# Kernel tuning notes

Hardware: AMD Instinct MI355X
Metric: run time of the kernel (lower is better)

The kernel has to match this reference:

```python
import jax, jax.numpy as jnp
import numpy as np

WS = 8          # window size
N = WS * WS     # tokens per window (64)
C = 256         # embed dim
H = 8           # heads
D = C // H      # head dim (32)
NW = 256        # windows per image
B_ = 2048       # total windows in batch (8 images * 256 windows)
CPB_HIDDEN = 512


def _make_relative_position_index():
    coords_h = np.arange(WS)
    coords_w = np.arange(WS)
    coords = np.stack(np.meshgrid(coords_h, coords_w, indexing='ij'))  # [2,WS,WS]
    coords = coords.reshape(2, -1)                                     # [2,N]
    rel = coords[:, :, None] - coords[:, None, :]                      # [2,N,N]
    rel = rel.transpose(1, 2, 0).astype(np.int64)                      # [N,N,2]
    rel[:, :, 0] += WS - 1
    rel[:, :, 1] += WS - 1
    rel[:, :, 0] *= 2 * WS - 1
    return rel.sum(-1)                                                 # [N,N]


def _make_relative_coords_table():
    rh = np.arange(-(WS - 1), WS, dtype=np.float64)
    rw = np.arange(-(WS - 1), WS, dtype=np.float64)
    tbl = np.stack(np.meshgrid(rh, rw, indexing='ij')).transpose(1, 2, 0)[None]  # [1,2W-1,2W-1,2]
    tbl[:, :, :, 0] /= (WS - 1)  # pretrained_window_size == window_size
    tbl[:, :, :, 1] /= (WS - 1)
    tbl *= 8
    tbl = np.sign(tbl) * np.log2(np.abs(tbl) + 1.0) / np.log2(8)
    return tbl.astype(np.float32)


def setup_inputs() -> dict:
    key = jax.random.key(0)
    ks = jax.random.split(key, 8)
    x = jax.random.normal(ks[0], (B_, N, C), dtype=jnp.float32)
    # shifted-window style additive mask: 0 for allowed, -100 for masked
    mask_bits = jax.random.uniform(ks[1], (NW, N, N)) < 0.1
    mask = jnp.where(mask_bits, jnp.float32(-100.0), jnp.float32(0.0))
    qkv_w = jax.random.normal(ks[2], (C, 3 * C), dtype=jnp.float32) * (1.0 / np.sqrt(C))
    q_bias = jnp.zeros((C,), jnp.float32)
    v_bias = jnp.zeros((C,), jnp.float32)
    logit_scale = jnp.full((H, 1, 1), np.log(10.0), dtype=jnp.float32)
    coords_table = jnp.asarray(_make_relative_coords_table())
    mlp1_w = jax.random.normal(ks[3], (2, CPB_HIDDEN), dtype=jnp.float32) * 0.5
    mlp1_b = jnp.zeros((CPB_HIDDEN,), jnp.float32)
    mlp2_w = jax.random.normal(ks[4], (CPB_HIDDEN, H), dtype=jnp.float32) * (1.0 / np.sqrt(CPB_HIDDEN))
    proj_w = jax.random.normal(ks[5], (C, C), dtype=jnp.float32) * (1.0 / np.sqrt(C))
    proj_b = jnp.zeros((C,), jnp.float32)
    rel_pos_index = jnp.asarray(_make_relative_position_index())  # [N,N] int64
    return {
        'x': x, 'mask': mask, 'qkv_w': qkv_w, 'q_bias': q_bias, 'v_bias': v_bias,
        'logit_scale': logit_scale, 'coords_table': coords_table,
        'mlp1_w': mlp1_w, 'mlp1_b': mlp1_b, 'mlp2_w': mlp2_w,
        'proj_w': proj_w, 'proj_b': proj_b, 'rel_pos_index': rel_pos_index,
    }


def _l2norm(t, axis=-1, eps=1e-12):
    n = jnp.sqrt(jnp.sum(t * t, axis=axis, keepdims=True))
    return t / jnp.maximum(n, eps)


def reference(x, mask, qkv_w, q_bias, v_bias, logit_scale, coords_table,
              mlp1_w, mlp1_b, mlp2_w, proj_w, proj_b, rel_pos_index):
    b, n, c = x.shape
    # qkv projection with (q_bias, 0, v_bias)
    qkv_bias = jnp.concatenate([q_bias, jnp.zeros_like(v_bias), v_bias], axis=0)
    qkv = x @ qkv_w + qkv_bias                          # [b, n, 3c]
    qkv = qkv.reshape(b, n, 3, H, D).transpose(2, 0, 3, 1, 4)  # [3, b, H, n, D]
    q, k, v = qkv[0], qkv[1], qkv[2]
    # cosine attention with learned per-head logit scale
    attn = jnp.einsum('bhnd,bhmd->bhnm', _l2norm(q), _l2norm(k))
    scale = jnp.exp(jnp.minimum(logit_scale, jnp.float32(np.log(1.0 / 0.01))))  # [H,1,1]
    attn = attn * scale[None]                           # [b, H, n, n]
    # continuous position bias MLP
    hbt = jax.nn.relu(coords_table @ mlp1_w + mlp1_b)   # [1, 2W-1, 2W-1, 512]
    bias_table = (hbt @ mlp2_w).reshape(-1, H)          # [(2W-1)^2, H]
    rel_bias = bias_table[rel_pos_index.reshape(-1)].reshape(n, n, H)
    rel_bias = 16.0 * jax.nn.sigmoid(rel_bias.transpose(2, 0, 1))  # [H, n, n]
    attn = attn + rel_bias[None]
    # shifted-window mask
    nw = mask.shape[0]
    attn = attn.reshape(b // nw, nw, H, n, n) + mask[None, :, None]
    attn = attn.reshape(b, H, n, n)
    attn = jax.nn.softmax(attn, axis=-1)
    out = jnp.einsum('bhnm,bhmd->bnhd', attn, v).reshape(b, n, c)
    return out @ proj_w + proj_b
```

## Files before the change

kernel.cpp:

```cpp
#include <hip/hip_runtime.h>
#include <hip/hip_bf16.h>
#include <stdint.h>

#define NTOK   64
#define CDIM   256
#define NHEAD  8
#define DHEAD  32
#define NWIN   256
#define BWIN   2048
#define MROWS  131072

typedef __attribute__((ext_vector_type(8))) short short8;
typedef __attribute__((ext_vector_type(4))) float f32x4;

__device__ __forceinline__ ushort f2bf(float f) {
  uint32_t u = __float_as_uint(f);
  u += 0x7fffu + ((u >> 16) & 1u);
  return (ushort)(u >> 16);
}
__device__ __forceinline__ void unpack8(uint4 u, float* f) {
  f[0] = __uint_as_float(u.x << 16);
  f[1] = __uint_as_float(u.x & 0xffff0000u);
  f[2] = __uint_as_float(u.y << 16);
  f[3] = __uint_as_float(u.y & 0xffff0000u);
  f[4] = __uint_as_float(u.z << 16);
  f[5] = __uint_as_float(u.z & 0xffff0000u);
  f[6] = __uint_as_float(u.w << 16);
  f[7] = __uint_as_float(u.w & 0xffff0000u);
}


__global__ void k_cast_bf16(const float* __restrict__ src, ushort* __restrict__ dst, int n4) {
  int i = blockIdx.x * blockDim.x + threadIdx.x;
  int stride = gridDim.x * blockDim.x;
  for (; i < n4; i += stride) {
    float4 v = ((const float4*)src)[i];
    ushort4 o;
    o.x = f2bf(v.x); o.y = f2bf(v.y); o.z = f2bf(v.z); o.w = f2bf(v.w);
    ((ushort4*)dst)[i] = o;
  }
}

__global__ void k_transpose_bf16(const float* __restrict__ src, ushort* __restrict__ dst, int K, int N) {
  int idx = blockIdx.x * 256 + threadIdx.x;
  if (idx < N * K) {
    int n = idx / K, k = idx - n * K;
    dst[idx] = f2bf(src[(size_t)k * N + n]);
  }
}

__global__ void k_cpb(const float* __restrict__ ct, const float* __restrict__ w1,
                      const float* __restrict__ b1, const float* __restrict__ w2,
                      float* __restrict__ out) {
  int p = blockIdx.x, t = threadIdx.x;
  float c0 = ct[p * 2], c1 = ct[p * 2 + 1];
  float acc[8];
#pragma unroll
  for (int h = 0; h < 8; ++h) acc[h] = 0.f;
  for (int j = t; j < 512; j += 256) {
    float hj = fmaxf(0.f, fmaf(c0, w1[j], fmaf(c1, w1[512 + j], b1[j])));
#pragma unroll
    for (int h = 0; h < 8; ++h) acc[h] = fmaf(hj, w2[j * 8 + h], acc[h]);
  }
#pragma unroll
  for (int off = 1; off < 64; off <<= 1)
#pragma unroll
    for (int h = 0; h < 8; ++h) acc[h] += __shfl_xor(acc[h], off, 64);
  __shared__ float red[4][8];
  if ((t & 63) == 0)
#pragma unroll
    for (int h = 0; h < 8; ++h) red[t >> 6][h] = acc[h];
  __syncthreads();
  if (t < 8) out[p * 8 + t] = red[0][t] + red[1][t] + red[2][t] + red[3][t];
}

__global__ void k_relbC(const float* __restrict__ bt, const int* __restrict__ rpi,
                        float* __restrict__ out) {
  int idx = blockIdx.x * 256 + threadIdx.x;
  int reg = idx & 3, l16 = (idx >> 2) & 15, g = (idx >> 6) & 3;
  int mt = (idx >> 8) & 3, nt = (idx >> 10) & 3, h = idx >> 12;
  int q = mt * 16 + l16, k = nt * 16 + g * 4 + reg;
  float v = bt[rpi[q * 64 + k] * 8 + h];
  out[idx] = 16.0f / (1.0f + __expf(-v));
}

__global__ void k_maskBits(const float* __restrict__ mask, unsigned char* __restrict__ out) {
  int idx = blockIdx.x * 256 + threadIdx.x;
  int b = idx & 15;
  int q6 = (idx >> 4) & 63;
  int wi = idx >> 10;
  int nt = b >> 2, mt = b & 3, g = q6 >> 4, l16 = q6 & 15;
  unsigned char v = 0;
#pragma unroll
  for (int reg = 0; reg < 4; ++reg) {
    int q = mt * 16 + l16, k = nt * 16 + g * 4 + reg;
    if (mask[(size_t)wi * 4096 + q * 64 + k] == 0.0f) v |= (unsigned char)(1 << reg);
  }
  out[idx] = v;
}

template <int MODE>
__global__ __launch_bounds__(256, 2) void gemm_bt(const ushort* __restrict__ A,
                                                  const ushort* __restrict__ BT,
                                                  void* __restrict__ Cout,
                                                  const float* __restrict__ bias0,
                                                  const float* __restrict__ bias1,
                                                  int K, int N) {
  __shared__ ushort As[128 * 64];
  __shared__ ushort Bs[128 * 64];
  const int t = threadIdx.x;
  const int bn = blockIdx.x, bm = blockIdx.y;
  const int wv = t >> 6, lane = t & 63, quad = lane >> 4, l16 = lane & 15;
  const int mbase = (wv & 1) * 64, nbase = (wv >> 1) * 64;

  f32x4 acc[4][4] = {};

  const int nkt = K >> 6;
  for (int kt = 0; kt < nkt; ++kt) {
    __syncthreads();
#pragma unroll
    for (int i = 0; i < 4; ++i) {
      int idx = i * 256 + t;
      int m = idx >> 3, c = idx & 7;
      int sw = (m * 8 + (c ^ (m & 7))) * 8;
      *(uint4*)(As + sw) = *(const uint4*)(A + (size_t)(bm * 128 + m) * K + kt * 64 + c * 8);
      *(uint4*)(Bs + sw) = *(const uint4*)(BT + (size_t)(bn * 128 + m) * K + kt * 64 + c * 8);
    }
    __syncthreads();
#pragma unroll
    for (int k2 = 0; k2 < 2; ++k2) {
      const int cidx = (k2 * 4 + quad) ^ (l16 & 7);
      short8 a[4], b[4];
#pragma unroll
      for (int mt = 0; mt < 4; ++mt)
        a[mt] = *(const short8*)(As + ((mbase + mt * 16 + l16) * 8 + cidx) * 8);
#pragma unroll
      for (int nt = 0; nt < 4; ++nt)
        b[nt] = *(const short8*)(Bs + ((nbase + nt * 16 + l16) * 8 + cidx) * 8);
#pragma unroll
      for (int mt = 0; mt < 4; ++mt)
#pragma unroll
        for (int nt = 0; nt < 4; ++nt)
          acc[mt][nt] = __builtin_amdgcn_mfma_f32_16x16x32_bf16(a[mt], b[nt], acc[mt][nt], 0, 0, 0);
    }
  }

#pragma unroll
  for (int mt = 0; mt < 4; ++mt)
#pragma unroll
    for (int nt = 0; nt < 4; ++nt) {
      int j = bn * 128 + nbase + nt * 16 + l16;
      int gm = bm * 128 + mbase + mt * 16 + quad * 4;
      float bs;
      if (MODE == 0) bs = (j < 256) ? bias0[j] : ((j < 512) ? 0.0f : bias1[j - 512]);
      else bs = bias0[j];
#pragma unroll
      for (int i2 = 0; i2 < 4; ++i2) {
        float v = acc[mt][nt][i2] + bs;
        size_t off = (size_t)(gm + i2) * N + j;
        if (MODE == 0) ((ushort*)Cout)[off] = f2bf(v);
        else ((float*)Cout)[off] = v;
      }
    }
}

__global__ __launch_bounds__(256, 2) void k_attn_mfma(const ushort* __restrict__ qkv,
                                                      const unsigned char* __restrict__ maskN,
                                                      const float* __restrict__ ls,
                                                      const float* __restrict__ relbC,
                                                      ushort* __restrict__ aob) {
  __shared__ ushort Vt[4][32][72];
  __shared__ ushort Ps[4][64][72];
  const int b = blockIdx.x, t = threadIdx.x;
  const int wi = b & (NWIN - 1);
  const int wv = t >> 6, lane = t & 63;
  const int g = lane >> 4, l16 = lane & 15;
  const size_t rowb = (size_t)b * 64;

  const uint4 mbits = *(const uint4*)(maskN + (size_t)wi * 1024 + (g * 16 + l16) * 16);
  const unsigned char* mb = (const unsigned char*)&mbits;

  for (int pass = 0; pass < 2; ++pass) {
    const int h = pass * 4 + wv;

    {
      const int tok = lane;
      const size_t base = (rowb + tok) * 768 + 512 + h * 32;
      union { uint4 u[4]; ushort s[32]; } raw;
      raw.u[0] = *(const uint4*)(qkv + base);
      raw.u[1] = *(const uint4*)(qkv + base + 8);
      raw.u[2] = *(const uint4*)(qkv + base + 16);
      raw.u[3] = *(const uint4*)(qkv + base + 24);
#pragma unroll
      for (int d = 0; d < 32; ++d) Vt[wv][d][tok] = raw.s[d];
    }

    const float sc = __expf(fminf(ls[h], 4.6051701859880914f));
    short8 qfr[4], kfr[4];
#pragma unroll
    for (int mt = 0; mt < 4; ++mt) {
      uint4 r = *(const uint4*)(qkv + (rowb + mt * 16 + l16) * 768 + h * 32 + g * 8);
      float f[8];
      unpack8(r, f);
      float s = 0.f;
#pragma unroll
      for (int j = 0; j < 8; ++j) s = fmaf(f[j], f[j], s);
      s += __shfl_xor(s, 16, 64);
      s += __shfl_xor(s, 32, 64);
      const float fac = sc / fmaxf(sqrtf(s), 1e-12f);
      union { short8 v; ushort us[8]; } o;
#pragma unroll
      for (int j = 0; j < 8; ++j) o.us[j] = f2bf(f[j] * fac);
      qfr[mt] = o.v;
    }
#pragma unroll
    for (int nt = 0; nt < 4; ++nt) {
      uint4 r = *(const uint4*)(qkv + (rowb + nt * 16 + l16) * 768 + 256 + h * 32 + g * 8);
      float f[8];
      unpack8(r, f);
      float s = 0.f;
#pragma unroll
      for (int j = 0; j < 8; ++j) s = fmaf(f[j], f[j], s);
      s += __shfl_xor(s, 16, 64);
      s += __shfl_xor(s, 32, 64);
      const float fac = 1.0f / fmaxf(sqrtf(s), 1e-12f);
      union { short8 v; ushort us[8]; } o;
#pragma unroll
      for (int j = 0; j < 8; ++j) o.us[j] = f2bf(f[j] * fac);
      kfr[nt] = o.v;
    }

    f32x4 sv[4][4];
    const f32x4 zero = {0.f, 0.f, 0.f, 0.f};
#pragma unroll
    for (int nt = 0; nt < 4; ++nt)
#pragma unroll
      for (int mt = 0; mt < 4; ++mt)
        sv[nt][mt] = __builtin_amdgcn_mfma_f32_16x16x32_bf16(kfr[nt], qfr[mt], zero, 0, 0, 0);

#pragma unroll
    for (int nt = 0; nt < 4; ++nt)
#pragma unroll
      for (int mt = 0; mt < 4; ++mt) {
        float4 rb = *(const float4*)(relbC + (size_t)(((h * 4 + nt) * 4 + mt) * 4 + g) * 64 + l16 * 4);
        const unsigned char nb = mb[nt * 4 + mt];
        sv[nt][mt][0] += rb.x + ((nb & 1) ? 0.f : -100.f);
        sv[nt][mt][1] += rb.y + ((nb & 2) ? 0.f : -100.f);
        sv[nt][mt][2] += rb.z + ((nb & 4) ? 0.f : -100.f);
        sv[nt][mt][3] += rb.w + ((nb & 8) ? 0.f : -100.f);
      }

#pragma unroll
    for (int mt = 0; mt < 4; ++mt) {
      float m = sv[0][mt][0];
#pragma unroll
      for (int nt = 0; nt < 4; ++nt)
#pragma unroll
        for (int reg = 0; reg < 4; ++reg) m = fmaxf(m, sv[nt][mt][reg]);
      m = fmaxf(m, __shfl_xor(m, 16, 64));
      m = fmaxf(m, __shfl_xor(m, 32, 64));
      float s = 0.f;
#pragma unroll
      for (int nt = 0; nt < 4; ++nt)
#pragma unroll
        for (int reg = 0; reg < 4; ++reg) {
          float e = __expf(sv[nt][mt][reg] - m);
          sv[nt][mt][reg] = e;
          s += e;
        }
      s += __shfl_xor(s, 16, 64);
      s += __shfl_xor(s, 32, 64);
      const float iv = 1.0f / s;
#pragma unroll
      for (int nt = 0; nt < 4; ++nt) {
        uint2 u;
        u.x = (uint32_t)f2bf(sv[nt][mt][0] * iv) | ((uint32_t)f2bf(sv[nt][mt][1] * iv) << 16);
        u.y = (uint32_t)f2bf(sv[nt][mt][2] * iv) | ((uint32_t)f2bf(sv[nt][mt][3] * iv) << 16);
        *(uint2*)&Ps[wv][mt * 16 + l16][nt * 16 + g * 4] = u;
      }
    }

    f32x4 ov[4][2] = {};
#pragma unroll
    for (int kt = 0; kt < 2; ++kt) {
      short8 pf[4], vf[2];
#pragma unroll
      for (int mt = 0; mt < 4; ++mt) pf[mt] = *(const short8*)&Ps[wv][mt * 16 + l16][kt * 32 + g * 8];
#pragma unroll
      for (int n2 = 0; n2 < 2; ++n2) vf[n2] = *(const short8*)&Vt[wv][n2 * 16 + l16][kt * 32 + g * 8];
#pragma unroll
      for (int mt = 0; mt < 4; ++mt)
#pragma unroll
        for (int n2 = 0; n2 < 2; ++n2)
          ov[mt][n2] = __builtin_amdgcn_mfma_f32_16x16x32_bf16(pf[mt], vf[n2], ov[mt][n2], 0, 0, 0);
    }

#pragma unroll
    for (int mt = 0; mt < 4; ++mt)
#pragma unroll
      for (int n2 = 0; n2 < 2; ++n2)
#pragma unroll
        for (int reg = 0; reg < 4; ++reg) {
          int r = mt * 16 + g * 4 + reg;
          aob[((size_t)b * 64 + r) * 256 + h * 32 + n2 * 16 + l16] = f2bf(ov[mt][n2][reg]);
        }
  }
}


extern "C" void kernel_launch(void* const* d_in, const int* in_sizes, int n_in,
                              void* d_out, int out_size, void* d_ws, size_t ws_size,
                              hipStream_t stream) {
  const float* x      = (const float*)d_in[0];
  const float* mask   = (const float*)d_in[1];
  const float* qkv_w  = (const float*)d_in[2];
  const float* q_bias = (const float*)d_in[3];
  const float* v_bias = (const float*)d_in[4];
  const float* lscale = (const float*)d_in[5];
  const float* ctbl   = (const float*)d_in[6];
  const float* m1w    = (const float*)d_in[7];
  const float* m1b    = (const float*)d_in[8];
  const float* m2w    = (const float*)d_in[9];
  const float* projw  = (const float*)d_in[10];
  const float* projb  = (const float*)d_in[11];
  const int*   rpi    = (const int*)d_in[12];

  char* w = (char*)d_ws;
  float*  bias_table = (float*)(w + 0);
  float*  relbC      = (float*)(w + 8192);
  unsigned char* maskN = (unsigned char*)(w + 139264);
  ushort* qkvWT      = (ushort*)(w + 4333568);
  ushort* projWT     = (ushort*)(w + 4726784);
  ushort* xb         = (ushort*)(w + 4857856);
  ushort* qkvb       = (ushort*)(w + 71966720ull);
  ushort* aob        = (ushort*)(w + 273293312ull);
  (void)ws_size; (void)n_in; (void)in_sizes; (void)out_size;

  k_cast_bf16<<<4096, 256, 0, stream>>>(x, xb, MROWS * CDIM / 4);
  k_transpose_bf16<<<768, 256, 0, stream>>>(qkv_w, qkvWT, 256, 768);
  k_transpose_bf16<<<256, 256, 0, stream>>>(projw, projWT, 256, 256);
  k_cpb<<<225, 256, 0, stream>>>(ctbl, m1w, m1b, m2w, bias_table);
  k_relbC<<<128, 256, 0, stream>>>(bias_table, rpi, relbC);
  k_maskBits<<<1024, 256, 0, stream>>>(mask, maskN);

  gemm_bt<0><<<dim3(6, 1024), 256, 0, stream>>>(xb, qkvWT, qkvb, q_bias, v_bias, 256, 768);
  k_attn_mfma<<<BWIN, 256, 0, stream>>>(qkvb, maskN, lscale, relbC, aob);
  gemm_bt<1><<<dim3(2, 1024), 256, 0, stream>>>(aob, projWT, d_out, projb, nullptr, 256, 256);
}
```

Before: 526.7 us.

## Process attention per 16-row query tile to cut registers and LDS

Restructures the attention kernel to handle one 16-row query tile at a time: compute the scores, apply softmax, write the P tile to a smaller LDS buffer, then run the PV MFMAs. The V fragments are loaded once per head ahead of the loop. This shrinks the live score accumulators from 4x4 to 4 vectors and reduces the Ps LDS allocation by a factor of four. Launch bounds are raised to 3 blocks per SM so the freed resources can go to occupancy. In exchange, each tile serialises its dependency chain, which leaves less instruction-level parallelism inside a wave.

```diff
diff --git a/kernel.cpp b/kernel.cpp
--- a/kernel.cpp
+++ b/kernel.cpp
@@ -164,13 +164,13 @@
     }
 }
 
-__global__ __launch_bounds__(256, 2) void k_attn_mfma(const ushort* __restrict__ qkv,
+__global__ __launch_bounds__(256, 3) void k_attn_mfma(const ushort* __restrict__ qkv,
                                                       const unsigned char* __restrict__ maskN,
                                                       const float* __restrict__ ls,
                                                       const float* __restrict__ relbC,
                                                       ushort* __restrict__ aob) {
   __shared__ ushort Vt[4][32][72];
-  __shared__ ushort Ps[4][64][72];
+  __shared__ ushort Ps[4][16][72];
   const int b = blockIdx.x, t = threadIdx.x;
   const int wi = b & (NWIN - 1);
   const int wv = t >> 6, lane = t & 63;
@@ -196,23 +196,7 @@
     }
 
     const float sc = __expf(fminf(ls[h], 4.6051701859880914f));
-    short8 qfr[4], kfr[4];
-#pragma unroll
-    for (int mt = 0; mt < 4; ++mt) {
-      uint4 r = *(const uint4*)(qkv + (rowb + mt * 16 + l16) * 768 + h * 32 + g * 8);
-      float f[8];
-      unpack8(r, f);
-      float s = 0.f;
-#pragma unroll
-      for (int j = 0; j < 8; ++j) s = fmaf(f[j], f[j], s);
-      s += __shfl_xor(s, 16, 64);
-      s += __shfl_xor(s, 32, 64);
-      const float fac = sc / fmaxf(sqrtf(s), 1e-12f);
-      union { short8 v; ushort us[8]; } o;
-#pragma unroll
-      for (int j = 0; j < 8; ++j) o.us[j] = f2bf(f[j] * fac);
-      qfr[mt] = o.v;
-    }
+    short8 kfr[4];
 #pragma unroll
     for (int nt = 0; nt < 4; ++nt) {
       uint4 r = *(const uint4*)(qkv + (rowb + nt * 16 + l16) * 768 + 256 + h * 32 + g * 8);
@@ -230,33 +214,54 @@
       kfr[nt] = o.v;
     }
 
-    f32x4 sv[4][4];
+    short8 vf[2][2];
+#pragma unroll
+    for (int kt = 0; kt < 2; ++kt)
+#pragma unroll
+      for (int n2 = 0; n2 < 2; ++n2)
+        vf[kt][n2] = *(const short8*)&Vt[wv][n2 * 16 + l16][kt * 32 + g * 8];
+
     const f32x4 zero = {0.f, 0.f, 0.f, 0.f};
-#pragma unroll
-    for (int nt = 0; nt < 4; ++nt)
-#pragma unroll
-      for (int mt = 0; mt < 4; ++mt)
-        sv[nt][mt] = __builtin_amdgcn_mfma_f32_16x16x32_bf16(kfr[nt], qfr[mt], zero, 0, 0, 0);
-
-#pragma unroll
-    for (int nt = 0; nt < 4; ++nt)
-#pragma unroll
-      for (int mt = 0; mt < 4; ++mt) {
+
+#pragma unroll
+    for (int mt = 0; mt < 4; ++mt) {
+      short8 qfr;
+      {
+        uint4 r = *(const uint4*)(qkv + (rowb + mt * 16 + l16) * 768 + h * 32 + g * 8);
+        float f[8];
+        unpack8(r, f);
+        float s = 0.f;
+#pragma unroll
+        for (int j = 0; j < 8; ++j) s = fmaf(f[j], f[j], s);
+        s += __shfl_xor(s, 16, 64);
+        s += __shfl_xor(s, 32, 64);
+        const float fac = sc / fmaxf(sqrtf(s), 1e-12f);
+        union { short8 v; ushort us[8]; } o;
+#pragma unroll
+        for (int j = 0; j < 8; ++j) o.us[j] = f2bf(f[j] * fac);
+        qfr = o.v;
+      }
+
+      f32x4 sv[4];
+#pragma unroll
+      for (int nt = 0; nt < 4; ++nt)
+        sv[nt] = __builtin_amdgcn_mfma_f32_16x16x32_bf16(kfr[nt], qfr, zero, 0, 0, 0);
+
+#pragma unroll
+      for (int nt = 0; nt < 4; ++nt) {
         float4 rb = *(const float4*)(relbC + (size_t)(((h * 4 + nt) * 4 + mt) * 4 + g) * 64 + l16 * 4);
         const unsigned char nb = mb[nt * 4 + mt];
-        sv[nt][mt][0] += rb.x + ((nb & 1) ? 0.f : -100.f);
-        sv[nt][mt][1] += rb.y + ((nb & 2) ? 0.f : -100.f);
-        sv[nt][mt][2] += rb.z + ((nb & 4) ? 0.f : -100.f);
-        sv[nt][mt][3] += rb.w + ((nb & 8) ? 0.f : -100.f);
-      }
-
-#pragma unroll
-    for (int mt = 0; mt < 4; ++mt) {
-      float m = sv[0][mt][0];
+        sv[nt][0] += rb.x + ((nb & 1) ? 0.f : -100.f);
+        sv[nt][1] += rb.y + ((nb & 2) ? 0.f : -100.f);
+        sv[nt][2] += rb.z + ((nb & 4) ? 0.f : -100.f);
+        sv[nt][3] += rb.w + ((nb & 8) ? 0.f : -100.f);
+      }
+
+      float m = sv[0][0];
 #pragma unroll
       for (int nt = 0; nt < 4; ++nt)
 #pragma unroll
-        for (int reg = 0; reg < 4; ++reg) m = fmaxf(m, sv[nt][mt][reg]);
+        for (int reg = 0; reg < 4; ++reg) m = fmaxf(m, sv[nt][reg]);
       m = fmaxf(m, __shfl_xor(m, 16, 64));
       m = fmaxf(m, __shfl_xor(m, 32, 64));
       float s = 0.f;
@@ -264,46 +269,37 @@
       for (int nt = 0; nt < 4; ++nt)
 #pragma unroll
         for (int reg = 0; reg < 4; ++reg) {
-          float e = __expf(sv[nt][mt][reg] - m);
-          sv[nt][mt][reg] = e;
+          float e = __expf(sv[nt][reg] - m);
+          sv[nt][reg] = e;
           s += e;
         }
       s += __shfl_xor(s, 16, 64);
       s += __shfl_xor(s, 32, 64);
       const float iv = 1.0f / s;
+
 #pragma unroll
       for (int nt = 0; nt < 4; ++nt) {
         uint2 u;
-        u.x = (uint32_t)f2bf(sv[nt][mt][0] * iv) | ((uint32_t)f2bf(sv[nt][mt][1] * iv) << 16);
-        u.y = (uint32_t)f2bf(sv[nt][mt][2] * iv) | ((uint32_t)f2bf(sv[nt][mt][3] * iv) << 16);
-        *(uint2*)&Ps[wv][mt * 16 + l16][nt * 16 + g * 4] = u;
-      }
-    }
-
-    f32x4 ov[4][2] = {};
-#pragma unroll
-    for (int kt = 0; kt < 2; ++kt) {
-      short8 pf[4], vf[2];
-#pragma unroll
-      for (int mt = 0; mt < 4; ++mt) pf[mt] = *(const short8*)&Ps[wv][mt * 16 + l16][kt * 32 + g * 8];
-#pragma unroll
-      for (int n2 = 0; n2 < 2; ++n2) vf[n2] = *(const short8*)&Vt[wv][n2 * 16 + l16][kt * 32 + g * 8];
-#pragma unroll
-      for (int mt = 0; mt < 4; ++mt)
-#pragma unroll
-        for (int n2 = 0; n2 < 2; ++n2)
-          ov[mt][n2] = __builtin_amdgcn_mfma_f32_16x16x32_bf16(pf[mt], vf[n2], ov[mt][n2], 0, 0, 0);
-    }
-
-#pragma unroll
-    for (int mt = 0; mt < 4; ++mt)
-#pragma unroll
-      for (int n2 = 0; n2 < 2; ++n2)
+        u.x = (uint32_t)f2bf(sv[nt][0] * iv) | ((uint32_t)f2bf(sv[nt][1] * iv) << 16);
+        u.y = (uint32_t)f2bf(sv[nt][2] * iv) | ((uint32_t)f2bf(sv[nt][3] * iv) << 16);
+        *(uint2*)&Ps[wv][l16][nt * 16 + g * 4] = u;
+      }
+
+      {
+        short8 pf0 = *(const short8*)&Ps[wv][l16][g * 8];
+        short8 pf1 = *(const short8*)&Ps[wv][l16][32 + g * 8];
+        f32x4 ovA = __builtin_amdgcn_mfma_f32_16x16x32_bf16(pf0, vf[0][0], zero, 0, 0, 0);
+        f32x4 ovB = __builtin_amdgcn_mfma_f32_16x16x32_bf16(pf0, vf[0][1], zero, 0, 0, 0);
+        ovA = __builtin_amdgcn_mfma_f32_16x16x32_bf16(pf1, vf[1][0], ovA, 0, 0, 0);
+        ovB = __builtin_amdgcn_mfma_f32_16x16x32_bf16(pf1, vf[1][1], ovB, 0, 0, 0);
 #pragma unroll
         for (int reg = 0; reg < 4; ++reg) {
           int r = mt * 16 + g * 4 + reg;
-          aob[((size_t)b * 64 + r) * 256 + h * 32 + n2 * 16 + l16] = f2bf(ov[mt][n2][reg]);
+          aob[(rowb + r) * 256 + h * 32 + l16] = f2bf(ovA[reg]);
+          aob[(rowb + r) * 256 + h * 32 + 16 + l16] = f2bf(ovB[reg]);
         }
+      }
+    }
   }
 }
 
```

After: 552.7 us. 1.05x slower.
